# Optimization experiments

Measured on AMD Instinct MI355X. Metric: run time of the kernel, lower is better.

## Reference

```python
import jax, jax.numpy as jnp
import numpy as np

NUM_HEADS = 16
NUM_GROUPS = 4
NUM_KV_HEADS = NUM_HEADS // NUM_GROUPS  # 4
HEAD_DIM = 64
MAX_DIST = 484


def setup_inputs() -> dict:
    key = jax.random.key(0)
    ks = jax.random.split(key, 8)
    B, S, E, H = 32, 484, 1024, 1024
    kv_dim = HEAD_DIM * NUM_GROUPS  # 256
    s_in = 0.03
    return {
        "query": jax.random.normal(ks[0], (B, S, E), dtype=jnp.float32),
        "key": jax.random.normal(ks[1], (B, S, E), dtype=jnp.float32),
        "value": jax.random.normal(ks[2], (B, S, E), dtype=jnp.float32),
        "Wq": jax.random.normal(ks[3], (E, H), dtype=jnp.float32) * s_in,
        "Wk": jax.random.normal(ks[4], (E, kv_dim), dtype=jnp.float32) * s_in,
        "Wv": jax.random.normal(ks[5], (E, kv_dim), dtype=jnp.float32) * s_in,
        "Wo": jax.random.normal(ks[6], (H, E), dtype=jnp.float32) * s_in,
        "rel_table": jax.random.normal(ks[7], (2 * MAX_DIST - 1, NUM_HEADS), dtype=jnp.float32) * 0.02,
    }


def _rel_bias(rel_table, q_len, k_len):
    # relative position k - q, clipped to [-(MD-1), MD-1], shifted to table index
    rel = jnp.arange(k_len)[None, :] - jnp.arange(q_len)[:, None]
    idx = jnp.clip(rel, -(MAX_DIST - 1), MAX_DIST - 1) + (MAX_DIST - 1)
    bias = rel_table[idx]  # [q, k, heads]
    return jnp.transpose(bias, (2, 0, 1))  # [heads, q, k]


def reference(query, key, value, Wq, Wk, Wv, Wo, rel_table):
    B, Q, _ = query.shape
    K = key.shape[1]
    G, Hkv, D = NUM_GROUPS, NUM_KV_HEADS, HEAD_DIM
    # projections; torch head split: head index = g*Hkv + h
    q = (query @ Wq).reshape(B, Q, G * Hkv, D).transpose(0, 2, 1, 3)
    q = q.reshape(B, G, Hkv, Q, D)  # b g h sq d
    k = (key @ Wk).reshape(B, K, G, D).transpose(0, 2, 1, 3)  # b g sk d
    v = (value @ Wv).reshape(B, K, G, D).transpose(0, 2, 1, 3)  # b g sv d
    scale = jnp.float32(D) ** 0.5
    scores = jnp.einsum('bghqd,bgkd->bghqk', q, k) / scale
    bias = _rel_bias(rel_table, Q, K).reshape(1, G, Hkv, Q, K)
    attn = jax.nn.softmax(scores + bias, axis=-1)
    out = jnp.einsum('bghqk,bgkd->bghqd', attn, v)
    out = out.reshape(B, G * Hkv, Q, D).transpose(0, 2, 1, 3).reshape(B, Q, G * Hkv * D)
    return out @ Wo
```

## Files before the change

### kernel.cpp

```cpp
#include <hip/hip_runtime.h>
#include <hip/hip_bf16.h>

typedef __attribute__((ext_vector_type(8))) short short8;
typedef __attribute__((ext_vector_type(4))) float f32x4;
typedef __attribute__((ext_vector_type(4))) unsigned uintx4;

#define B_  32
#define S_  484
#define E_  1024
#define NH  16
#define SP  512
#define M_  (B_*S_)

static __device__ __forceinline__ ushort f2bf(float f) {
  union { float f; unsigned u; } v; v.f = f;
  unsigned u = v.u;
  return (ushort)((u + 0x7FFFu + ((u >> 16) & 1u)) >> 16);
}

static __device__ __forceinline__ unsigned cvt_pk_bf16(float lo, float hi) {
  unsigned r;
  asm("v_cvt_pk_bf16_f32 %0, %1, %2" : "=v"(r) : "v"(lo), "v"(hi));
  return r;
}

#define GLOAD_LDS16(gp, lp) \
  __builtin_amdgcn_global_load_lds((const __attribute__((address_space(1))) void*)(gp), \
                                   (__attribute__((address_space(3))) void*)(lp), 16, 0, 0)

__global__ __launch_bounds__(256)
void cvt_f32_bf16(const float* __restrict__ x, ushort* __restrict__ y, int n4) {
  int i = blockIdx.x * 256 + threadIdx.x;
  int stride = gridDim.x * 256;
  for (; i < n4; i += stride) {
    float4 v = ((const float4*)x)[i];
    ushort4 h;
    h.x = f2bf(v.x); h.y = f2bf(v.y); h.z = f2bf(v.z); h.w = f2bf(v.w);
    ((ushort4*)y)[i] = h;
  }
}

__global__ __launch_bounds__(256)
void transpose_all(const float* __restrict__ Wq, const float* __restrict__ Wk,
                   const float* __restrict__ Wv, const float* __restrict__ Wo,
                   ushort* __restrict__ wqT, ushort* __restrict__ wkT,
                   ushort* __restrict__ wvT, ushort* __restrict__ woT) {
  __shared__ float tile[32][33];
  int t = blockIdx.x;
  const float* W; ushort* WT; int N;
  if (t < 1024)      { W = Wq; WT = wqT; N = 1024; }
  else if (t < 1280) { W = Wk; WT = wkT; N = 256;  t -= 1024; }
  else if (t < 1536) { W = Wv; WT = wvT; N = 256;  t -= 1280; }
  else               { W = Wo; WT = woT; N = 1024; t -= 1536; }
  const int nx = N >> 5;
  const int n0 = (t % nx) * 32, k0 = (t / nx) * 32;
  const int tx = threadIdx.x & 31, ty = threadIdx.x >> 5;
  for (int i = ty; i < 32; i += 8) tile[i][tx] = W[(size_t)(k0 + i) * N + n0 + tx];
  __syncthreads();
  for (int i = ty; i < 32; i += 8) WT[(size_t)(n0 + i) * 1024 + k0 + tx] = f2bf(tile[tx][i]);
}

template<int EPI>
__global__ __launch_bounds__(512)
void gemm_cnt256(const ushort* __restrict__ A, const ushort* __restrict__ BT,
                 void* __restrict__ Cout, float oscale) {
  const int K = 1024, N = 1024, NK = 32;
  __shared__ alignas(16) ushort sA[4][256 * 32];
  __shared__ alignas(16) ushort sB[4][256 * 32];
  const int tid = threadIdx.x;
  const int lane = tid & 63, w = tid >> 6;

  const int nwg = gridDim.x;
  const int qq = nwg >> 3, rr = nwg & 7;
  const int x = blockIdx.x & 7, seq = blockIdx.x >> 3;
  const int logical = x * qq + (x < rr ? x : rr) + seq;
  const int m0 = (logical >> 2) * 256;
  const int n0 = (logical & 3) * 256;

  const int brow = tid >> 2;
  const int scol = (((tid & 3) ^ ((tid >> 3) & 3))) * 8;
  const int rowA0 = min(m0 + brow, M_ - 1);
  const int rowA1 = min(m0 + brow + 128, M_ - 1);
  const ushort* gA0 = A + (size_t)rowA0 * K + scol;
  const ushort* gA1 = A + (size_t)rowA1 * K + scol;
  const ushort* gB0 = BT + (size_t)(n0 + brow) * K + scol;
  const int dst = tid * 8;

  const int wr = w >> 2, wc = w & 3;
  const int g4 = lane >> 4, l16 = lane & 15;
  const int rs = (l16 >> 1) & 3;

  f32x4 acc[8][4] = {};

  auto stage = [&](int kt, int buf) {
    GLOAD_LDS16(gA0 + kt * 32,           &sA[buf][dst]);
    GLOAD_LDS16(gA1 + kt * 32,           &sA[buf][dst + 4096]);
    GLOAD_LDS16(gB0 + kt * 32,           &sB[buf][dst]);
    GLOAD_LDS16(gB0 + kt * 32 + 128 * K, &sB[buf][dst + 4096]);
  };

  stage(0, 0);
  stage(1, 1);
  stage(2, 2);

  int cur = 0;
  for (int kt = 0; kt < NK; ++kt) {
    if (kt < NK - 2)       asm volatile("s_waitcnt vmcnt(8)" ::: "memory");
    else if (kt == NK - 2) asm volatile("s_waitcnt vmcnt(4)" ::: "memory");
    else                   asm volatile("s_waitcnt vmcnt(0)" ::: "memory");
    asm volatile("s_waitcnt lgkmcnt(0)" ::: "memory");
    __builtin_amdgcn_s_barrier();
    if (kt + 3 < NK) stage(kt + 3, (cur + 3) & 3);
    const ushort* pa = &sA[cur][(wr * 128 + l16) * 32 + 8 * (g4 ^ rs)];
    const ushort* pb = &sB[cur][(wc * 64 + l16) * 32 + 8 * (g4 ^ rs)];
    short8 af[8], bf[4];
#pragma unroll
    for (int i = 0; i < 8; ++i) af[i] = *(const short8*)(pa + i * 16 * 32);
#pragma unroll
    for (int i = 0; i < 4; ++i) bf[i] = *(const short8*)(pb + i * 16 * 32);
#pragma unroll
    for (int mi = 0; mi < 8; ++mi)
#pragma unroll
      for (int ni = 0; ni < 4; ++ni)
        acc[mi][ni] = __builtin_amdgcn_mfma_f32_16x16x32_bf16(af[mi], bf[ni], acc[mi][ni], 0, 0, 0);
    cur = (cur + 1) & 3;
  }

#pragma unroll
  for (int mi = 0; mi < 8; ++mi) {
#pragma unroll
    for (int ni = 0; ni < 4; ++ni) {
#pragma unroll
      for (int r = 0; r < 4; ++r) {
        int m = m0 + wr * 128 + mi * 16 + g4 * 4 + r;
        int n = n0 + wc * 64 + ni * 16 + l16;
        if (m < M_) {
          float vv = acc[mi][ni][r];
          if (EPI == 2) {
            ((float*)Cout)[(size_t)m * N + n] = vv;
          } else {
            int b = m / S_, pos = m % S_;
            ushort hv = f2bf(vv * oscale);
            ((ushort*)Cout)[(((size_t)b * NH + (n >> 6)) * SP + pos) * 64 + (n & 63)] = hv;
          }
        }
      }
    }
  }
}

__global__ __launch_bounds__(256)
void kvproj(const float* __restrict__ key, const float* __restrict__ value,
            const ushort* __restrict__ wkT, const ushort* __restrict__ wvT,
            ushort* __restrict__ kp, ushort* __restrict__ vp) {
  const int K = 1024, NK = 32;
  __shared__ alignas(16) ushort sA[2][128 * 32];
  __shared__ alignas(16) ushort sB[2][128 * 32];
  const int tid = threadIdx.x;
  const int lane = tid & 63, w = tid >> 6;

  const int nwg = gridDim.x;
  const int qq = nwg >> 3, rr = nwg & 7;
  const int x = blockIdx.x & 7, seq = blockIdx.x >> 3;
  const int logical = x * qq + (x < rr ? x : rr) + seq;
  const bool isV = logical >= 242;
  const int l2 = isV ? logical - 242 : logical;
  const int m0 = (l2 >> 1) * 128;
  const int n0 = (l2 & 1) * 128;
  const float* Ain = isV ? value : key;
  const ushort* BT = isV ? wvT : wkT;
  ushort* Cout = isV ? vp : kp;

  const int srow = w * 32 + (lane >> 2);
  const int scol = ((lane & 3) ^ ((lane >> 3) & 3)) * 8;
  const ushort* gB0 = BT + (size_t)(n0 + srow) * K + scol;
  const int dstB = srow * 32 + (lane & 3) * 8;

  const int arow = w * 32 + (lane >> 1);
  const int acol = (lane & 1) * 16;
  const int sw = (lane >> 2) & 3;
  const int ag0 = (2 * (lane & 1)) ^ sw;
  const int ag1 = (2 * (lane & 1) + 1) ^ sw;
  const float* gA0f = Ain + (size_t)(m0 + arow) * K + acol;

  const int wr = w >> 1, wc = w & 1;
  const int g4 = lane >> 4, l16 = lane & 15;
  const int rsw = (l16 >> 1) & 3;
  const int aoff = (wr * 64 + l16) * 32 + 8 * (g4 ^ rsw);
  const int boff = (wc * 64 + l16) * 32 + 8 * (g4 ^ rsw);

  f32x4 acc[4][4] = {};
  float4 fA0, fA1, fA2, fA3;

  auto issueA = [&](int kt) {
    const float4* p = (const float4*)(gA0f + kt * 32);
    fA0 = p[0]; fA1 = p[1]; fA2 = p[2]; fA3 = p[3];
  };
  auto writeA = [&](int buf) {
    unsigned d0 = cvt_pk_bf16(fA0.x, fA0.y), d1 = cvt_pk_bf16(fA0.z, fA0.w);
    unsigned d2 = cvt_pk_bf16(fA1.x, fA1.y), d3 = cvt_pk_bf16(fA1.z, fA1.w);
    unsigned d4 = cvt_pk_bf16(fA2.x, fA2.y), d5 = cvt_pk_bf16(fA2.z, fA2.w);
    unsigned d6 = cvt_pk_bf16(fA3.x, fA3.y), d7 = cvt_pk_bf16(fA3.z, fA3.w);
    ushort* base = &sA[buf][arow * 32];
    uintx4 q0 = {d0, d1, d2, d3}, q1 = {d4, d5, d6, d7};
    *(uintx4*)(base + ag0 * 8) = q0;
    *(uintx4*)(base + ag1 * 8) = q1;
  };

  issueA(0);
  GLOAD_LDS16(gB0,          &sB[0][dstB]);
  GLOAD_LDS16(gB0 + 16 * K, &sB[0][dstB + 16 * 32]);
  writeA(0);

  for (int kt = 0; kt < NK; ++kt) {
    __syncthreads();
    const int nb = (kt + 1) & 1;
    if (kt + 1 < NK) {
      const ushort* gb = gB0 + (kt + 1) * 32;
      GLOAD_LDS16(gb,          &sB[nb][dstB]);
      GLOAD_LDS16(gb + 16 * K, &sB[nb][dstB + 16 * 32]);
      issueA(kt + 1);
    }
    const ushort* pa = &sA[kt & 1][aoff];
    const ushort* pb = &sB[kt & 1][boff];
    short8 af[4], bf[4];
#pragma unroll
    for (int i = 0; i < 4; ++i) {
      af[i] = *(const short8*)(pa + i * 16 * 32);
      bf[i] = *(const short8*)(pb + i * 16 * 32);
    }
#pragma unroll
    for (int mi = 0; mi < 4; ++mi)
#pragma unroll
      for (int ni = 0; ni < 4; ++ni)
        acc[mi][ni] = __builtin_amdgcn_mfma_f32_16x16x32_bf16(af[mi], bf[ni], acc[mi][ni], 0, 0, 0);
    if (kt + 1 < NK) writeA(nb);
  }

#pragma unroll
  for (int mi = 0; mi < 4; ++mi) {
#pragma unroll
    for (int ni = 0; ni < 4; ++ni) {
#pragma unroll
      for (int r = 0; r < 4; ++r) {
        int m = m0 + wr * 64 + mi * 16 + g4 * 4 + r;
        int n = n0 + wc * 64 + ni * 16 + l16;
        float vv = acc[mi][ni][r];
        int b = m / S_, pos = m % S_;
        if (!isV) {
          int dd = (n & 63) ^ ((pos & 7) << 3);
          Cout[(((size_t)b * 4 + (n >> 6)) * SP + pos) * 64 + dd] = f2bf(vv);
        } else {
          int local = pos & 31;
          int j = (local < 16) ? (2 * local) : (2 * local - 31);
          int pf_ = (pos & ~31) | (j ^ ((n & 3) << 3));
          Cout[(((size_t)b * 4 + (n >> 6)) * 64 + (n & 63)) * SP + pf_] = f2bf(vv);
        }
      }
    }
  }
}

__global__ __launch_bounds__(256)
void attn_kernel(const ushort* __restrict__ qp, const ushort* __restrict__ kp,
                 const ushort* __restrict__ vpT, const float* __restrict__ rel,
                 ushort* __restrict__ ao) {
  __shared__ float2 sBiasP[1056];
  __shared__ alignas(16) ushort sK[2][32 * 64];
  __shared__ alignas(16) ushort sV[2][64 * 32];
  __shared__ alignas(16) ushort sP[4][32 * 40];
  const int tid = threadIdx.x;
  const int blk = blockIdx.x;
  const int logical = (blk & 7) * 256 + (blk >> 3);
  const int qt = logical & 3, head = (logical >> 2) & 15, b = logical >> 6;
  const int g = head >> 2;
  const float LOG2E = 1.44269504f;
  for (int t = tid; t < 1056; t += 256) {
    float b0 = (t >= 32 && t < 999) ? rel[(t - 32) * 16 + head] * LOG2E : -1e30f;
    int t2 = t + 16;
    float b1 = (t2 >= 32 && t2 < 999) ? rel[(t2 - 32) * 16 + head] * LOG2E : -1e30f;
    sBiasP[t] = make_float2(b0, b1);
  }

  const int lane = tid & 63, w = tid >> 6;
  const int g4 = lane >> 4, l16 = lane & 15;
  const int qw = qt * 128 + w * 32;

  const ushort* qbA = qp + (((size_t)b * NH + head) * SP + qw + l16) * 64;
  const ushort* qbB = qbA + 16 * 64;
  short8 qf0a = *(const short8*)(qbA + 8 * g4);
  short8 qf1a = *(const short8*)(qbA + 32 + 8 * g4);
  short8 qf0b = *(const short8*)(qbB + 8 * g4);
  short8 qf1b = *(const short8*)(qbB + 32 + 8 * g4);

  const ushort* kSrc = kp  + ((size_t)b * 4 + g) * SP * 64 + (tid >> 3) * 64 + (tid & 7) * 8;
  const ushort* vSrc = vpT + ((size_t)b * 4 + g) * 64 * SP + (tid >> 2) * SP + (tid & 3) * 8;

  f32x4 accA[4] = {}, accB[4] = {};
  float psA[4] = {0.f, 0.f, 0.f, 0.f}, psB[4] = {0.f, 0.f, 0.f, 0.f};
  const int ibA = l16 - (qw + g4 * 4) + 515;
  const int ibB = ibA - 16;
  ushort* sPw = &sP[w][0];

  const int kswz  = (l16 & 7) << 3;
  const int kOff0 = l16 * 64 + ((8 * g4) ^ kswz);
  const int kOff1 = l16 * 64 + ((32 + 8 * g4) ^ kswz);
  const int vOff  = l16 * 32 + 8 * (g4 ^ (l16 & 3));

  GLOAD_LDS16(kSrc, &sK[0][w * 512]);
  GLOAD_LDS16(vSrc, &sV[0][w * 512]);

  for (int kt = 0; kt < 16; ++kt) {
    __syncthreads();
    if (kt + 1 < 16) {
      GLOAD_LDS16(kSrc + (kt + 1) * 2048, &sK[(kt + 1) & 1][w * 512]);
      GLOAD_LDS16(vSrc + (kt + 1) * 32,   &sV[(kt + 1) & 1][w * 512]);
    }
    const int k0 = kt * 32;
    float2 a0 = sBiasP[ibA + k0],     a1 = sBiasP[ibA + k0 - 1];
    float2 a2 = sBiasP[ibA + k0 - 2], a3 = sBiasP[ibA + k0 - 3];
    float2 c0 = sBiasP[ibB + k0],     c1 = sBiasP[ibB + k0 - 1];
    float2 c2 = sBiasP[ibB + k0 - 2], c3 = sBiasP[ibB + k0 - 3];
    f32x4 s0a = {a0.x, a1.x, a2.x, a3.x}, s1a = {a0.y, a1.y, a2.y, a3.y};
    f32x4 s0b = {c0.x, c1.x, c2.x, c3.x}, s1b = {c0.y, c1.y, c2.y, c3.y};

    const ushort* sk = &sK[kt & 1][0];
    const ushort* sv = &sV[kt & 1][0];
    short8 kf0 = *(const short8*)(sk + kOff0);
    short8 kf1 = *(const short8*)(sk + kOff1);
    short8 kf2 = *(const short8*)(sk + 1024 + kOff0);
    short8 kf3 = *(const short8*)(sk + 1024 + kOff1);
    s0a = __builtin_amdgcn_mfma_f32_16x16x32_bf16(qf0a, kf0, s0a, 0, 0, 0);
    s0a = __builtin_amdgcn_mfma_f32_16x16x32_bf16(qf1a, kf1, s0a, 0, 0, 0);
    s1a = __builtin_amdgcn_mfma_f32_16x16x32_bf16(qf0a, kf2, s1a, 0, 0, 0);
    s1a = __builtin_amdgcn_mfma_f32_16x16x32_bf16(qf1a, kf3, s1a, 0, 0, 0);
    s0b = __builtin_amdgcn_mfma_f32_16x16x32_bf16(qf0b, kf0, s0b, 0, 0, 0);
    s0b = __builtin_amdgcn_mfma_f32_16x16x32_bf16(qf1b, kf1, s0b, 0, 0, 0);
    s1b = __builtin_amdgcn_mfma_f32_16x16x32_bf16(qf0b, kf2, s1b, 0, 0, 0);
    s1b = __builtin_amdgcn_mfma_f32_16x16x32_bf16(qf1b, kf3, s1b, 0, 0, 0);

#pragma unroll
    for (int r = 0; r < 4; ++r) {
      float p0 = __builtin_amdgcn_exp2f(s0a[r]);
      float p1 = __builtin_amdgcn_exp2f(s1a[r]);
      float u0 = __builtin_amdgcn_exp2f(s0b[r]);
      float u1 = __builtin_amdgcn_exp2f(s1b[r]);
      if (kt == 15) {
        bool m0v = (k0 + l16 < S_), m1v = (k0 + 16 + l16 < S_);
        p0 = m0v ? p0 : 0.f;  p1 = m1v ? p1 : 0.f;
        u0 = m0v ? u0 : 0.f;  u1 = m1v ? u1 : 0.f;
      }
      psA[r] += p0 + p1;
      psB[r] += u0 + u1;
      *(unsigned*)(sPw + (g4 * 4 + r) * 40 + 2 * l16)        = cvt_pk_bf16(p0, p1);
      *(unsigned*)(sPw + (16 + g4 * 4 + r) * 40 + 2 * l16)   = cvt_pk_bf16(u0, u1);
    }
    short8 pfA = *(const short8*)(sPw + l16 * 40 + 8 * g4);
    short8 pfB = *(const short8*)(sPw + (16 + l16) * 40 + 8 * g4);
#pragma unroll
    for (int nt = 0; nt < 4; ++nt) {
      short8 vf = *(const short8*)(sv + vOff + nt * 512);
      accA[nt] = __builtin_amdgcn_mfma_f32_16x16x32_bf16(pfA, vf, accA[nt], 0, 0, 0);
      accB[nt] = __builtin_amdgcn_mfma_f32_16x16x32_bf16(pfB, vf, accB[nt], 0, 0, 0);
    }
  }

#pragma unroll
  for (int off = 1; off < 16; off <<= 1) {
#pragma unroll
    for (int r = 0; r < 4; ++r) {
      psA[r] += __shfl_xor(psA[r], off, 64);
      psB[r] += __shfl_xor(psB[r], off, 64);
    }
  }

#pragma unroll
  for (int r = 0; r < 4; ++r) {
    int qa = qw + g4 * 4 + r;
    if (qa < S_) {
      float inv = 1.f / psA[r];
#pragma unroll
      for (int nt = 0; nt < 4; ++nt)
        ao[((size_t)b * S_ + qa) * 1024 + head * 64 + nt * 16 + l16] = f2bf(accA[nt][r] * inv);
    }
    int qb2 = qa + 16;
    if (qb2 < S_) {
      float inv = 1.f / psB[r];
#pragma unroll
      for (int nt = 0; nt < 4; ++nt)
        ao[((size_t)b * S_ + qb2) * 1024 + head * 64 + nt * 16 + l16] = f2bf(accB[nt][r] * inv);
    }
  }
}

extern "C" void kernel_launch(void* const* d_in, const int* in_sizes, int n_in,
                              void* d_out, int out_size, void* d_ws, size_t ws_size,
                              hipStream_t stream) {
  const float* query = (const float*)d_in[0];
  const float* key   = (const float*)d_in[1];
  const float* value = (const float*)d_in[2];
  const float* Wq    = (const float*)d_in[3];
  const float* Wk    = (const float*)d_in[4];
  const float* Wv    = (const float*)d_in[5];
  const float* Wo    = (const float*)d_in[6];
  const float* rel   = (const float*)d_in[7];

  char* ws = (char*)d_ws;
  size_t off = 0;
  auto alloc = [&](size_t bytes) { char* p = ws + off; off += (bytes + 255) & ~(size_t)255; return p; };

  const size_t MEelems = (size_t)M_ * E_;
  ushort* qb  = (ushort*)alloc(MEelems * 2);
  ushort* wqT = (ushort*)alloc((size_t)1024 * 1024 * 2);
  ushort* wkT = (ushort*)alloc((size_t)256 * 1024 * 2);
  ushort* wvT = (ushort*)alloc((size_t)256 * 1024 * 2);
  ushort* woT = (ushort*)alloc((size_t)1024 * 1024 * 2);
  ushort* qp  = (ushort*)alloc((size_t)B_ * NH * SP * 64 * 2);
  ushort* kp  = (ushort*)alloc((size_t)B_ * 4 * SP * 64 * 2);
  ushort* vp  = (ushort*)alloc((size_t)B_ * 4 * 64 * SP * 2);
  ushort* ao  = (ushort*)alloc(MEelems * 2);

  cvt_f32_bf16<<<2048, 256, 0, stream>>>(query, qb, (int)(MEelems / 4));

  transpose_all<<<2560, 256, 0, stream>>>(Wq, Wk, Wv, Wo, wqT, wkT, wvT, woT);

  const float QSCALE = 0.125f * 1.44269504f;
  gemm_cnt256<0><<<244, 512, 0, stream>>>(qb, wqT, qp, QSCALE);
  kvproj<<<484, 256, 0, stream>>>(key, value, wkT, wvT, kp, vp);

  attn_kernel<<<2048, 256, 0, stream>>>(qp, kp, vp, rel, ao);

  gemm_cnt256<2><<<244, 512, 0, stream>>>(ao, woT, d_out, 1.0f);
}
```

Before: 256.4 us.

## Enlarge KV projection tiles to 256x256 with a four-stage pipelined loop

The K/V projection kernel goes from 484 workgroups of 256 threads with 128x128 tiles to 122 workgroups of 512 threads, each computing a 256x256 tile. The main loop becomes a four-buffer, three-deep prefetch pipeline with explicit vmcnt/lgkmcnt waits and raw barriers in place of __syncthreads. It relies on wkT and wvT being adjacent in the workspace, so one pointer with n0=256 reaches the V weights. The aim is better operand reuse and more latency hiding. The cost is only 122 workgroups on a GPU with many more CUs, plus 128KB of LDS per workgroup, which lowers occupancy.

```diff
diff --git a/kernel.cpp b/kernel.cpp
--- a/kernel.cpp
+++ b/kernel.cpp
@@ -149,13 +149,13 @@
   }
 }
 
-__global__ __launch_bounds__(256)
-void kvproj(const float* __restrict__ key, const float* __restrict__ value,
-            const ushort* __restrict__ wkT, const ushort* __restrict__ wvT,
-            ushort* __restrict__ kp, ushort* __restrict__ vp) {
+__global__ __launch_bounds__(512)
+void kvproj256(const float* __restrict__ key, const float* __restrict__ value,
+               const ushort* __restrict__ BT,
+               ushort* __restrict__ kp, ushort* __restrict__ vp) {
   const int K = 1024, NK = 32;
-  __shared__ alignas(16) ushort sA[2][128 * 32];
-  __shared__ alignas(16) ushort sB[2][128 * 32];
+  __shared__ alignas(16) ushort sA[4][256 * 32];
+  __shared__ alignas(16) ushort sB[4][256 * 32];
   const int tid = threadIdx.x;
   const int lane = tid & 63, w = tid >> 6;
 
@@ -163,98 +163,114 @@
   const int qq = nwg >> 3, rr = nwg & 7;
   const int x = blockIdx.x & 7, seq = blockIdx.x >> 3;
   const int logical = x * qq + (x < rr ? x : rr) + seq;
-  const bool isV = logical >= 242;
-  const int l2 = isV ? logical - 242 : logical;
-  const int m0 = (l2 >> 1) * 128;
-  const int n0 = (l2 & 1) * 128;
+  const int m0 = (logical >> 1) * 256;
+  const bool isV = (logical & 1) != 0;
+  const int n0 = isV ? 256 : 0;
   const float* Ain = isV ? value : key;
-  const ushort* BT = isV ? wvT : wkT;
-  ushort* Cout = isV ? vp : kp;
-
-  const int srow = w * 32 + (lane >> 2);
-  const int scol = ((lane & 3) ^ ((lane >> 3) & 3)) * 8;
-  const ushort* gB0 = BT + (size_t)(n0 + srow) * K + scol;
-  const int dstB = srow * 32 + (lane & 3) * 8;
-
-  const int arow = w * 32 + (lane >> 1);
-  const int acol = (lane & 1) * 16;
-  const int sw = (lane >> 2) & 3;
-  const int ag0 = (2 * (lane & 1)) ^ sw;
-  const int ag1 = (2 * (lane & 1) + 1) ^ sw;
-  const float* gA0f = Ain + (size_t)(m0 + arow) * K + acol;
-
-  const int wr = w >> 1, wc = w & 1;
+
+  const int brow = tid >> 2;
+  const int scol = (((tid & 3) ^ ((tid >> 3) & 3))) * 8;
+  const ushort* gB0 = BT + (size_t)(n0 + brow) * K + scol;
+  const int dstB = tid * 8;
+
+  const int arow = tid >> 1;
+  const int rowAf = min(m0 + arow, M_ - 1);
+  const float* gAf = Ain + (size_t)rowAf * K + (tid & 1) * 16;
+  const int sw = (arow >> 1) & 3;
+  const int ag0 = (2 * (tid & 1)) ^ sw;
+  const int ag1 = (2 * (tid & 1) + 1) ^ sw;
+
+  const int wr = w >> 2, wc = w & 3;
   const int g4 = lane >> 4, l16 = lane & 15;
-  const int rsw = (l16 >> 1) & 3;
-  const int aoff = (wr * 64 + l16) * 32 + 8 * (g4 ^ rsw);
-  const int boff = (wc * 64 + l16) * 32 + 8 * (g4 ^ rsw);
-
-  f32x4 acc[4][4] = {};
-  float4 fA0, fA1, fA2, fA3;
-
-  auto issueA = [&](int kt) {
-    const float4* p = (const float4*)(gA0f + kt * 32);
-    fA0 = p[0]; fA1 = p[1]; fA2 = p[2]; fA3 = p[3];
+  const int rs = (l16 >> 1) & 3;
+
+  f32x4 acc[8][4] = {};
+  float4 fA[3][4];
+
+  auto stageB = [&](int kt) {
+    int buf = kt & 3;
+    GLOAD_LDS16(gB0 + kt * 32,           &sB[buf][dstB]);
+    GLOAD_LDS16(gB0 + kt * 32 + 128 * K, &sB[buf][dstB + 4096]);
   };
-  auto writeA = [&](int buf) {
-    unsigned d0 = cvt_pk_bf16(fA0.x, fA0.y), d1 = cvt_pk_bf16(fA0.z, fA0.w);
-    unsigned d2 = cvt_pk_bf16(fA1.x, fA1.y), d3 = cvt_pk_bf16(fA1.z, fA1.w);
-    unsigned d4 = cvt_pk_bf16(fA2.x, fA2.y), d5 = cvt_pk_bf16(fA2.z, fA2.w);
-    unsigned d6 = cvt_pk_bf16(fA3.x, fA3.y), d7 = cvt_pk_bf16(fA3.z, fA3.w);
-    ushort* base = &sA[buf][arow * 32];
-    uintx4 q0 = {d0, d1, d2, d3}, q1 = {d4, d5, d6, d7};
-    *(uintx4*)(base + ag0 * 8) = q0;
-    *(uintx4*)(base + ag1 * 8) = q1;
-  };
-
-  issueA(0);
-  GLOAD_LDS16(gB0,          &sB[0][dstB]);
-  GLOAD_LDS16(gB0 + 16 * K, &sB[0][dstB + 16 * 32]);
-  writeA(0);
-
-  for (int kt = 0; kt < NK; ++kt) {
-    __syncthreads();
-    const int nb = (kt + 1) & 1;
-    if (kt + 1 < NK) {
-      const ushort* gb = gB0 + (kt + 1) * 32;
-      GLOAD_LDS16(gb,          &sB[nb][dstB]);
-      GLOAD_LDS16(gb + 16 * K, &sB[nb][dstB + 16 * 32]);
-      issueA(kt + 1);
-    }
-    const ushort* pa = &sA[kt & 1][aoff];
-    const ushort* pb = &sB[kt & 1][boff];
-    short8 af[4], bf[4];
-#pragma unroll
-    for (int i = 0; i < 4; ++i) {
-      af[i] = *(const short8*)(pa + i * 16 * 32);
-      bf[i] = *(const short8*)(pb + i * 16 * 32);
-    }
-#pragma unroll
-    for (int mi = 0; mi < 4; ++mi)
+  auto compute = [&](int kt) {
+    const int buf = kt & 3;
+    const ushort* pa = &sA[buf][(wr * 128 + l16) * 32 + 8 * (g4 ^ rs)];
+    const ushort* pb = &sB[buf][(wc * 64 + l16) * 32 + 8 * (g4 ^ rs)];
+    short8 af[8], bf[4];
+#pragma unroll
+    for (int i = 0; i < 8; ++i) af[i] = *(const short8*)(pa + i * 16 * 32);
+#pragma unroll
+    for (int i = 0; i < 4; ++i) bf[i] = *(const short8*)(pb + i * 16 * 32);
+#pragma unroll
+    for (int mi = 0; mi < 8; ++mi)
 #pragma unroll
       for (int ni = 0; ni < 4; ++ni)
         acc[mi][ni] = __builtin_amdgcn_mfma_f32_16x16x32_bf16(af[mi], bf[ni], acc[mi][ni], 0, 0, 0);
-    if (kt + 1 < NK) writeA(nb);
-  }
-
-#pragma unroll
-  for (int mi = 0; mi < 4; ++mi) {
+  };
+
+#define ISSUEA(kt, slot) do { \
+    const float4* _p = (const float4*)(gAf + (kt) * 32); \
+    fA[slot][0] = _p[0]; fA[slot][1] = _p[1]; fA[slot][2] = _p[2]; fA[slot][3] = _p[3]; \
+  } while (0)
+#define WRITEA(kt, slot) do { \
+    unsigned _d0 = cvt_pk_bf16(fA[slot][0].x, fA[slot][0].y), _d1 = cvt_pk_bf16(fA[slot][0].z, fA[slot][0].w); \
+    unsigned _d2 = cvt_pk_bf16(fA[slot][1].x, fA[slot][1].y), _d3 = cvt_pk_bf16(fA[slot][1].z, fA[slot][1].w); \
+    unsigned _d4 = cvt_pk_bf16(fA[slot][2].x, fA[slot][2].y), _d5 = cvt_pk_bf16(fA[slot][2].z, fA[slot][2].w); \
+    unsigned _d6 = cvt_pk_bf16(fA[slot][3].x, fA[slot][3].y), _d7 = cvt_pk_bf16(fA[slot][3].z, fA[slot][3].w); \
+    ushort* _base = &sA[(kt) & 3][arow * 32]; \
+    uintx4 _q0 = {_d0, _d1, _d2, _d3}, _q1 = {_d4, _d5, _d6, _d7}; \
+    *(uintx4*)(_base + ag0 * 8) = _q0; \
+    *(uintx4*)(_base + ag1 * 8) = _q1; \
+  } while (0)
+#define KSTEP(kt, ws, is) do { \
+    if ((kt) < NK - 2) asm volatile("s_waitcnt vmcnt(6)" ::: "memory"); \
+    else               asm volatile("s_waitcnt vmcnt(0)" ::: "memory"); \
+    if ((kt) + 1 < NK) WRITEA((kt) + 1, ws); \
+    asm volatile("s_waitcnt lgkmcnt(0)" ::: "memory"); \
+    __builtin_amdgcn_s_barrier(); \
+    if ((kt) + 3 < NK) { stageB((kt) + 3); ISSUEA((kt) + 3, is); } \
+    compute(kt); \
+  } while (0)
+
+  stageB(0); ISSUEA(0, 0);
+  stageB(1); ISSUEA(1, 1);
+  stageB(2); ISSUEA(2, 2);
+  asm volatile("s_waitcnt vmcnt(12)" ::: "memory");
+  WRITEA(0, 0);
+
+  for (int kb = 0; kb < 30; kb += 3) {
+    KSTEP(kb,     1, 0);
+    KSTEP(kb + 1, 2, 1);
+    KSTEP(kb + 2, 0, 2);
+  }
+  KSTEP(30, 1, 0);
+  KSTEP(31, 0, 0);
+
+#undef KSTEP
+#undef WRITEA
+#undef ISSUEA
+
+#pragma unroll
+  for (int mi = 0; mi < 8; ++mi) {
 #pragma unroll
     for (int ni = 0; ni < 4; ++ni) {
 #pragma unroll
       for (int r = 0; r < 4; ++r) {
-        int m = m0 + wr * 64 + mi * 16 + g4 * 4 + r;
-        int n = n0 + wc * 64 + ni * 16 + l16;
-        float vv = acc[mi][ni][r];
-        int b = m / S_, pos = m % S_;
-        if (!isV) {
-          int dd = (n & 63) ^ ((pos & 7) << 3);
-          Cout[(((size_t)b * 4 + (n >> 6)) * SP + pos) * 64 + dd] = f2bf(vv);
-        } else {
-          int local = pos & 31;
-          int j = (local < 16) ? (2 * local) : (2 * local - 31);
-          int pf_ = (pos & ~31) | (j ^ ((n & 3) << 3));
-          Cout[(((size_t)b * 4 + (n >> 6)) * 64 + (n & 63)) * SP + pf_] = f2bf(vv);
+        int m = m0 + wr * 128 + mi * 16 + g4 * 4 + r;
+        int nl = wc * 64 + ni * 16 + l16;
+        if (m < M_) {
+          float vv = acc[mi][ni][r];
+          int b = m / S_, pos = m % S_;
+          int h = nl >> 6, d = nl & 63;
+          if (!isV) {
+            int dd = d ^ ((pos & 7) << 3);
+            kp[(((size_t)b * 4 + h) * SP + pos) * 64 + dd] = f2bf(vv);
+          } else {
+            int local = pos & 31;
+            int j = (local < 16) ? (2 * local) : (2 * local - 31);
+            int pf_ = (pos & ~31) | (j ^ ((d & 3) << 3));
+            vp[(((size_t)b * 4 + h) * 64 + d) * SP + pf_] = f2bf(vv);
+          }
         }
       }
     }
@@ -419,6 +435,7 @@
   ushort* kp  = (ushort*)alloc((size_t)B_ * 4 * SP * 64 * 2);
   ushort* vp  = (ushort*)alloc((size_t)B_ * 4 * 64 * SP * 2);
   ushort* ao  = (ushort*)alloc(MEelems * 2);
+  (void)wvT;
 
   cvt_f32_bf16<<<2048, 256, 0, stream>>>(query, qb, (int)(MEelems / 4));
 
@@ -426,7 +443,7 @@
 
   const float QSCALE = 0.125f * 1.44269504f;
   gemm_cnt256<0><<<244, 512, 0, stream>>>(qb, wqT, qp, QSCALE);
-  kvproj<<<484, 256, 0, stream>>>(key, value, wkT, wvT, kp, vp);
+  kvproj256<<<122, 512, 0, stream>>>(key, value, wkT, kp, vp);
 
   attn_kernel<<<2048, 256, 0, stream>>>(qp, kp, vp, rel, ao);
 
```

After: 284.1 us. +10.8%, slower.
